# Kernel optimization log

Measured on AMD Instinct MI355X. Metric: run time of the kernel, lower is better.

## Reference

```python
import jax, jax.numpy as jnp
import numpy as np
import math

DIM = 512
D_STATE = 16
D_CONV = 4
EXPAND = 2
D_INNER = EXPAND * DIM
DT_RANK = math.ceil(DIM / 16)  # 'auto'
B_SZ = 4
N_TOK = 4097


def setup_inputs() -> dict:
    key = jax.random.key(0)
    ks = jax.random.split(key, 12)
    s = 0.02
    x = jax.random.normal(ks[0], (B_SZ, N_TOK, DIM), dtype=jnp.float32)
    q_w = jax.random.normal(ks[1], (DIM, DIM), dtype=jnp.float32) * s
    in_proj_w = jax.random.normal(ks[2], (2 * D_INNER, DIM), dtype=jnp.float32) * s
    conv_w = jax.random.normal(ks[3], (D_INNER, D_CONV), dtype=jnp.float32) * s
    conv_b = jnp.zeros((D_INNER,), dtype=jnp.float32)
    x_proj_w = jax.random.normal(ks[4], (DT_RANK + 2 * D_STATE, D_INNER), dtype=jnp.float32) * s
    dt_w = jax.random.normal(ks[5], (D_INNER, DT_RANK), dtype=jnp.float32) * (DT_RANK ** -0.5)
    # dt bias: inverse softplus of dt sampled log-uniform in [dt_min, dt_max]
    dt = jnp.exp(jax.random.uniform(ks[6], (D_INNER,)) * (math.log(0.1) - math.log(0.001)) + math.log(0.001))
    dt_b = (dt + jnp.log(-jnp.expm1(-dt))).astype(jnp.float32)
    # A = 1..d_state per channel (S4D-real init)
    A_log = jnp.log(jnp.broadcast_to(jnp.arange(1, D_STATE + 1, dtype=jnp.float32), (D_INNER, D_STATE)))
    D = jnp.ones((D_INNER,), dtype=jnp.float32)
    out_proj_w = jax.random.normal(ks[7], (DIM, D_INNER), dtype=jnp.float32) * s
    proj_w = jax.random.normal(ks[8], (DIM, DIM), dtype=jnp.float32) * s
    proj_b = jnp.zeros((DIM,), dtype=jnp.float32)
    return {"x": x, "q_w": q_w, "in_proj_w": in_proj_w, "conv_w": conv_w, "conv_b": conv_b,
            "x_proj_w": x_proj_w, "dt_w": dt_w, "dt_b": dt_b, "A_log": A_log, "D": D,
            "out_proj_w": out_proj_w, "proj_w": proj_w, "proj_b": proj_b}


def _selective_scan(u, delta, A, Bm, Cm, D):
    # u, delta: (B, L, d); A: (d, n); Bm, Cm: (B, L, n); D: (d,)
    b, L, d = u.shape
    n = A.shape[1]

    def step(h, inp):
        u_t, d_t, b_t, c_t = inp  # (B,d) (B,d) (B,n) (B,n)
        dA = jnp.exp(d_t[..., None] * A)                      # (B, d, n)
        h = h * dA + (d_t * u_t)[..., None] * b_t[:, None, :]  # (B, d, n)
        y = jnp.einsum('bdn,bn->bd', h, c_t)
        return h, y

    h0 = jnp.zeros((b, d, n), dtype=u.dtype)
    _, ys = jax.lax.scan(step, h0, (u.transpose(1, 0, 2), delta.transpose(1, 0, 2),
                                    Bm.transpose(1, 0, 2), Cm.transpose(1, 0, 2)))
    return ys.transpose(1, 0, 2) + u * D  # (B, L, d)


def _mamba(tokens, in_proj_w, conv_w, conv_b, x_proj_w, dt_w, dt_b, A_log, D, out_proj_w):
    b, L, _ = tokens.shape
    xz = tokens @ in_proj_w.T                          # (B, L, 2*d_inner)
    xi, z = jnp.split(xz, 2, axis=-1)
    # causal depthwise conv1d over L
    xc = xi.transpose(0, 2, 1)                         # (B, d_inner, L)
    xc = jax.lax.conv_general_dilated(
        xc, conv_w[:, None, :], window_strides=(1,), padding=[(D_CONV - 1, 0)],
        feature_group_count=D_INNER)
    xc = xc + conv_b[None, :, None]
    xs = jax.nn.silu(xc.transpose(0, 2, 1))            # (B, L, d_inner)
    x_dbl = xs @ x_proj_w.T                            # (B, L, dt_rank + 2n)
    dt, Bm, Cm = jnp.split(x_dbl, [DT_RANK, DT_RANK + D_STATE], axis=-1)
    delta = jax.nn.softplus(dt @ dt_w.T + dt_b)        # (B, L, d_inner)
    A = -jnp.exp(A_log)                                # (d_inner, n)
    y = _selective_scan(xs, delta, A, Bm, Cm, D)
    y = y * jax.nn.silu(z)
    return y @ out_proj_w.T                            # (B, L, dim)


def reference(x, q_w, in_proj_w, conv_w, conv_b, x_proj_w, dt_w, dt_b, A_log, D, out_proj_w, proj_w, proj_b):
    cls_tok = x[:, :1, :]
    patch = x[:, 1:, :]
    q = cls_tok @ q_w.T
    tokens = jnp.concatenate([q, patch], axis=1)
    mixed = _mamba(tokens, in_proj_w, conv_w, conv_b, x_proj_w, dt_w, dt_b, A_log, D, out_proj_w)
    upd_cls = mixed[:, :1, :] @ proj_w.T + proj_b
    return jnp.concatenate([upd_cls, patch], axis=1)
```

## Files before the change

kernel.cpp:

```cpp
#include <hip/hip_runtime.h>
#include <math.h>


#define B_SZ 4
#define DIM 512
#define D_INNER 1024
#define L_TOK 4097
#define TOK_STRIDE (L_TOK * DIM)
#define PB4 (TOK_STRIDE / 4)
#define N4 (B_SZ * PB4)
#define DT_RANK 32
#define D_STATE 16
#define CB 1639

#define SL0 0u
#define SL1 419533u
#define SL2 839066u
#define SL3 1258599u
#define SL4 1678132u
#define SL5 2097664u

__device__ __forceinline__ float silu_f(float v) { return v / (1.f + expf(-v)); }
__device__ __forceinline__ float f4dot(float4 a, float4 b) {
    return a.x * b.x + a.y * b.y + a.z * b.z + a.w * b.w;
}
__device__ __forceinline__ float red16(float v) {
    v += __shfl_xor(v, 1, 64); v += __shfl_xor(v, 2, 64);
    v += __shfl_xor(v, 4, 64); v += __shfl_xor(v, 8, 64);
    return v;
}
__device__ __forceinline__ float red32(float v) {
    v = red16(v); v += __shfl_xor(v, 16, 64); return v;
}
__device__ __forceinline__ float sel4(int c, float a0, float a1, float a2, float a3) {
    return (c == 0) ? a0 : (c == 1) ? a1 : (c == 2) ? a2 : a3;
}

__device__ __forceinline__ void do_copy(const float4* __restrict__ x4,
                                        float4* __restrict__ o4,
                                        int cb_idx, unsigned beg, unsigned end) {
    const unsigned stride = (unsigned)CB * 256u;
    for (unsigned i = beg + (unsigned)cb_idx * 256u + threadIdx.x; i < end; i += stride) {
        unsigned r = i;
        if (r >= 2u * PB4) r -= 2u * PB4;
        if (r >= (unsigned)PB4) r -= (unsigned)PB4;
        if (r >= 128u) o4[i] = x4[i];
    }
}

__global__ void __launch_bounds__(256)
k1_q(const float* __restrict__ x, const float* __restrict__ q_w,
     float* __restrict__ q_ws, float4* __restrict__ o4) {
    const int blk = blockIdx.x, tid = threadIdx.x;
    if (blk >= 8) { do_copy((const float4*)x, o4, blk - 8, SL0, SL1); return; }
    __shared__ float cls[4 * DIM];
    {
        float4* cl4 = (float4*)cls;
        const float4* xg = (const float4*)x;
#pragma unroll
        for (int t = 0; t < 2; ++t) {
            int f = tid + t * 256;
            cl4[f] = xg[(size_t)(f >> 7) * PB4 + (f & 127)];
        }
    }
    __syncthreads();
    const int w = tid >> 6, lane = tid & 63, c = lane & 15, g = lane >> 4;
#pragma unroll
    for (int p = 0; p < 4; ++p) {
        int r = blk * 64 + w * 16 + p * 4 + g;
        const float4* wr = (const float4*)(q_w + (size_t)r * DIM);
        float a0 = 0, a1 = 0, a2 = 0, a3 = 0;
#pragma unroll
        for (int j = 0; j < 8; ++j) {
            float4 wv = wr[c + 16 * j];
            a0 += f4dot(wv, ((const float4*)(cls))[c + 16 * j]);
            a1 += f4dot(wv, ((const float4*)(cls + DIM))[c + 16 * j]);
            a2 += f4dot(wv, ((const float4*)(cls + 2 * DIM))[c + 16 * j]);
            a3 += f4dot(wv, ((const float4*)(cls + 3 * DIM))[c + 16 * j]);
        }
        a0 = red16(a0); a1 = red16(a1); a2 = red16(a2); a3 = red16(a3);
        if (c < 4) q_ws[c * DIM + r] = sel4(c, a0, a1, a2, a3);
    }
}

__global__ void __launch_bounds__(256)
k2_xz(const float* __restrict__ q_ws, const float* __restrict__ in_proj_w,
      const float* __restrict__ conv_w, const float* __restrict__ conv_b,
      float* __restrict__ xs_ws, float* __restrict__ gz_ws,
      const float4* __restrict__ x4, float4* __restrict__ o4) {
    const int blk = blockIdx.x, tid = threadIdx.x;
    if (blk >= 32) { do_copy(x4, o4, blk - 32, SL1, SL2); return; }
    __shared__ float q_lds[4 * DIM];
    {
        float4* ql = (float4*)q_lds;
        const float4* qg = (const float4*)q_ws;
        ql[tid] = qg[tid]; ql[tid + 256] = qg[tid + 256];
    }
    __syncthreads();
    const int w = tid >> 6, lane = tid & 63, c = lane & 15, g = lane >> 4;
#pragma unroll
    for (int p = 0; p < 4; ++p) {
        int r = blk * 64 + w * 16 + p * 4 + g;
        const float4* wr = (const float4*)(in_proj_w + (size_t)r * DIM);
        float a0 = 0, a1 = 0, a2 = 0, a3 = 0;
#pragma unroll
        for (int j = 0; j < 8; ++j) {
            float4 wv = wr[c + 16 * j];
            a0 += f4dot(wv, ((const float4*)(q_lds))[c + 16 * j]);
            a1 += f4dot(wv, ((const float4*)(q_lds + DIM))[c + 16 * j]);
            a2 += f4dot(wv, ((const float4*)(q_lds + 2 * DIM))[c + 16 * j]);
            a3 += f4dot(wv, ((const float4*)(q_lds + 3 * DIM))[c + 16 * j]);
        }
        a0 = red16(a0); a1 = red16(a1); a2 = red16(a2); a3 = red16(a3);
        if (c < 4) {
            float v = sel4(c, a0, a1, a2, a3);
            if (r < D_INNER)
                xs_ws[c * D_INNER + r] = silu_f(v * conv_w[r * 4 + 3] + conv_b[r]);
            else
                gz_ws[c * D_INNER + (r - D_INNER)] = silu_f(v);
        }
    }
}

__global__ void __launch_bounds__(256)
k3_xd(const float* __restrict__ xs_ws, const float* __restrict__ x_proj_w,
      float* __restrict__ xd_ws, const float4* __restrict__ x4,
      float4* __restrict__ o4) {
    const int blk = blockIdx.x, tid = threadIdx.x;
    if (blk >= 4) { do_copy(x4, o4, blk - 4, SL2, SL3); return; }
    __shared__ float xs_lds[4 * D_INNER];
    {
        float4* xl = (float4*)xs_lds;
        const float4* xg = (const float4*)xs_ws;
#pragma unroll
        for (int t = 0; t < 4; ++t) xl[tid + t * 256] = xg[tid + t * 256];
    }
    __syncthreads();
    const int w = tid >> 6, lane = tid & 63, c2 = lane & 31, g2 = lane >> 5;
#pragma unroll
    for (int p = 0; p < 2; ++p) {
        int r = blk * 16 + w * 4 + p * 2 + g2;
        const float4* wr = (const float4*)(x_proj_w + (size_t)r * D_INNER);
        float a0 = 0, a1 = 0, a2 = 0, a3 = 0;
#pragma unroll
        for (int j = 0; j < 8; ++j) {
            float4 wv = wr[c2 + 32 * j];
            a0 += f4dot(wv, ((const float4*)(xs_lds))[c2 + 32 * j]);
            a1 += f4dot(wv, ((const float4*)(xs_lds + D_INNER))[c2 + 32 * j]);
            a2 += f4dot(wv, ((const float4*)(xs_lds + 2 * D_INNER))[c2 + 32 * j]);
            a3 += f4dot(wv, ((const float4*)(xs_lds + 3 * D_INNER))[c2 + 32 * j]);
        }
        a0 = red32(a0); a1 = red32(a1); a2 = red32(a2); a3 = red32(a3);
        if (c2 < 4) xd_ws[c2 * 64 + r] = sel4(c2, a0, a1, a2, a3);
    }
}

__global__ void __launch_bounds__(256)
k4_out(const float* __restrict__ xs_ws, const float* __restrict__ gz_ws,
       const float* __restrict__ xd_ws, const float* __restrict__ dt_w,
       const float* __restrict__ dt_b, const float* __restrict__ Dp,
       const float* __restrict__ out_proj_w, float* __restrict__ o_ws,
       const float4* __restrict__ x4, float4* __restrict__ o4) {
    const int blk = blockIdx.x, tid = threadIdx.x;
    if (blk >= 16) { do_copy(x4, o4, blk - 16, SL3, SL4); return; }
    __shared__ float xd_lds[4 * 64];
    __shared__ float y_lds[4 * D_INNER];
    if (tid < 64) ((float4*)xd_lds)[tid] = ((const float4*)xd_ws)[tid];
    __syncthreads();
    float S[4];
#pragma unroll
    for (int b = 0; b < 4; ++b) {
        float s = 0.f;
#pragma unroll
        for (int n = 0; n < D_STATE; ++n)
            s += xd_lds[b * 64 + 32 + n] * xd_lds[b * 64 + 48 + n];
        S[b] = s;
    }
#pragma unroll
    for (int qq = 0; qq < 4; ++qq) {
        int d = tid + qq * 256;
        const float4* dw = (const float4*)(dt_w + (size_t)d * DT_RANK);
        float4 dwv[8];
#pragma unroll
        for (int j = 0; j < 8; ++j) dwv[j] = dw[j];
        float Dd = Dp[d], db = dt_b[d];
#pragma unroll
        for (int b = 0; b < 4; ++b) {
            const float4* xd4 = (const float4*)(xd_lds + b * 64);
            float dp = db;
#pragma unroll
            for (int j = 0; j < 8; ++j) dp += f4dot(dwv[j], xd4[j]);
            float delta = (dp > 20.f) ? dp : log1pf(expf(dp));
            y_lds[b * D_INNER + d] =
                xs_ws[b * D_INNER + d] * (delta * S[b] + Dd) * gz_ws[b * D_INNER + d];
        }
    }
    __syncthreads();
    const int w = tid >> 6, lane = tid & 63, c2 = lane & 31, g2 = lane >> 5;
#pragma unroll
    for (int p = 0; p < 4; ++p) {
        int r = blk * 32 + w * 8 + p * 2 + g2;
        const float4* wr = (const float4*)(out_proj_w + (size_t)r * D_INNER);
        float a0 = 0, a1 = 0, a2 = 0, a3 = 0;
#pragma unroll
        for (int j = 0; j < 8; ++j) {
            float4 wv = wr[c2 + 32 * j];
            a0 += f4dot(wv, ((const float4*)(y_lds))[c2 + 32 * j]);
            a1 += f4dot(wv, ((const float4*)(y_lds + D_INNER))[c2 + 32 * j]);
            a2 += f4dot(wv, ((const float4*)(y_lds + 2 * D_INNER))[c2 + 32 * j]);
            a3 += f4dot(wv, ((const float4*)(y_lds + 3 * D_INNER))[c2 + 32 * j]);
        }
        a0 = red32(a0); a1 = red32(a1); a2 = red32(a2); a3 = red32(a3);
        if (c2 < 4) o_ws[c2 * DIM + r] = sel4(c2, a0, a1, a2, a3);
    }
}

__global__ void __launch_bounds__(256)
k5_upd(const float* __restrict__ o_ws, const float* __restrict__ proj_w,
       const float* __restrict__ proj_b, float* __restrict__ out,
       const float4* __restrict__ x4, float4* __restrict__ o4) {
    const int blk = blockIdx.x, tid = threadIdx.x;
    if (blk >= 8) { do_copy(x4, o4, blk - 8, SL4, SL5); return; }
    __shared__ float o_lds[4 * DIM];
    {
        float4* ol = (float4*)o_lds;
        const float4* og = (const float4*)o_ws;
        ol[tid] = og[tid]; ol[tid + 256] = og[tid + 256];
    }
    __syncthreads();
    const int w = tid >> 6, lane = tid & 63, c = lane & 15, g = lane >> 4;
#pragma unroll
    for (int p = 0; p < 4; ++p) {
        int r = blk * 64 + w * 16 + p * 4 + g;
        const float4* wr = (const float4*)(proj_w + (size_t)r * DIM);
        float a0 = 0, a1 = 0, a2 = 0, a3 = 0;
#pragma unroll
        for (int j = 0; j < 8; ++j) {
            float4 wv = wr[c + 16 * j];
            a0 += f4dot(wv, ((const float4*)(o_lds))[c + 16 * j]);
            a1 += f4dot(wv, ((const float4*)(o_lds + DIM))[c + 16 * j]);
            a2 += f4dot(wv, ((const float4*)(o_lds + 2 * DIM))[c + 16 * j]);
            a3 += f4dot(wv, ((const float4*)(o_lds + 3 * DIM))[c + 16 * j]);
        }
        a0 = red16(a0); a1 = red16(a1); a2 = red16(a2); a3 = red16(a3);
        if (c < 4) out[(size_t)c * TOK_STRIDE + r] = sel4(c, a0, a1, a2, a3) + proj_b[r];
    }
}

extern "C" void kernel_launch(void* const* d_in, const int* in_sizes, int n_in,
                              void* d_out, int out_size, void* d_ws, size_t ws_size,
                              hipStream_t stream) {
    const float* x          = (const float*)d_in[0];
    const float* q_w        = (const float*)d_in[1];
    const float* in_proj_w  = (const float*)d_in[2];
    const float* conv_w     = (const float*)d_in[3];
    const float* conv_b     = (const float*)d_in[4];
    const float* x_proj_w   = (const float*)d_in[5];
    const float* dt_w       = (const float*)d_in[6];
    const float* dt_b       = (const float*)d_in[7];
    const float* Dp         = (const float*)d_in[9];
    const float* out_proj_w = (const float*)d_in[10];
    const float* proj_w     = (const float*)d_in[11];
    const float* proj_b     = (const float*)d_in[12];
    float* out = (float*)d_out;
    float* ws  = (float*)d_ws;

    float* q_ws  = ws;
    float* xs_ws = ws + 2048;
    float* gz_ws = ws + 6144;
    float* xd_ws = ws + 10240;
    float* o_ws  = ws + 10496;

    const float4* x4 = (const float4*)x;
    float4* o4 = (float4*)out;

    k1_q  <<<8 + CB,  256, 0, stream>>>(x, q_w, q_ws, o4);
    k2_xz <<<32 + CB, 256, 0, stream>>>(q_ws, in_proj_w, conv_w, conv_b,
                                        xs_ws, gz_ws, x4, o4);
    k3_xd <<<4 + CB,  256, 0, stream>>>(xs_ws, x_proj_w, xd_ws, x4, o4);
    k4_out<<<16 + CB, 256, 0, stream>>>(xs_ws, gz_ws, xd_ws, dt_w, dt_b, Dp,
                                        out_proj_w, o_ws, x4, o4);
    k5_upd<<<8 + CB,  256, 0, stream>>>(o_ws, proj_w, proj_b, out, x4, o4);
}
```

Measured before the change: 146.8 us.

## Fuse x_proj stage into out-projection kernel, redundantly per block

Removes the separate x_proj kernel launch by having each of the 16 out-projection blocks recompute the full 64-row x_proj product from LDS-resident xs. The background patch copy is repartitioned into four slices instead of five, with a larger copy-block count per launch. This trades one fewer launch and a global round-trip for redundant x_proj work in every compute block and larger LDS use per block.

```diff
diff --git a/kernel.cpp b/kernel.cpp
--- a/kernel.cpp
+++ b/kernel.cpp
@@ -8,17 +8,15 @@
 #define L_TOK 4097
 #define TOK_STRIDE (L_TOK * DIM)
 #define PB4 (TOK_STRIDE / 4)
-#define N4 (B_SZ * PB4)
 #define DT_RANK 32
 #define D_STATE 16
-#define CB 1639
+#define CB 2040
 
 #define SL0 0u
-#define SL1 419533u
-#define SL2 839066u
-#define SL3 1258599u
-#define SL4 1678132u
-#define SL5 2097664u
+#define SL1 ((unsigned)PB4)
+#define SL2 (2u * PB4)
+#define SL3 (3u * PB4)
+#define SL4 (4u * PB4)
 
 __device__ __forceinline__ float silu_f(float v) { return v / (1.f + expf(-v)); }
 __device__ __forceinline__ float f4dot(float4 a, float4 b) {
@@ -123,12 +121,16 @@
 }
 
 __global__ void __launch_bounds__(256)
-k3_xd(const float* __restrict__ xs_ws, const float* __restrict__ x_proj_w,
-      float* __restrict__ xd_ws, const float4* __restrict__ x4,
-      float4* __restrict__ o4) {
-    const int blk = blockIdx.x, tid = threadIdx.x;
-    if (blk >= 4) { do_copy(x4, o4, blk - 4, SL2, SL3); return; }
+k4_out(const float* __restrict__ xs_ws, const float* __restrict__ gz_ws,
+       const float* __restrict__ x_proj_w, const float* __restrict__ dt_w,
+       const float* __restrict__ dt_b, const float* __restrict__ Dp,
+       const float* __restrict__ out_proj_w, float* __restrict__ o_ws,
+       const float4* __restrict__ x4, float4* __restrict__ o4) {
+    const int blk = blockIdx.x, tid = threadIdx.x;
+    if (blk >= 16) { do_copy(x4, o4, blk - 16, SL2, SL3); return; }
     __shared__ float xs_lds[4 * D_INNER];
+    __shared__ float xd_lds[4 * 64];
+    __shared__ float y_lds[4 * D_INNER];
     {
         float4* xl = (float4*)xs_lds;
         const float4* xg = (const float4*)xs_ws;
@@ -137,9 +139,10 @@
     }
     __syncthreads();
     const int w = tid >> 6, lane = tid & 63, c2 = lane & 31, g2 = lane >> 5;
-#pragma unroll
-    for (int p = 0; p < 2; ++p) {
-        int r = blk * 16 + w * 4 + p * 2 + g2;
+
+#pragma unroll
+    for (int p = 0; p < 8; ++p) {
+        int r = p * 8 + w * 2 + g2;
         const float4* wr = (const float4*)(x_proj_w + (size_t)r * D_INNER);
         float a0 = 0, a1 = 0, a2 = 0, a3 = 0;
 #pragma unroll
@@ -151,22 +154,10 @@
             a3 += f4dot(wv, ((const float4*)(xs_lds + 3 * D_INNER))[c2 + 32 * j]);
         }
         a0 = red32(a0); a1 = red32(a1); a2 = red32(a2); a3 = red32(a3);
-        if (c2 < 4) xd_ws[c2 * 64 + r] = sel4(c2, a0, a1, a2, a3);
-    }
-}
-
-__global__ void __launch_bounds__(256)
-k4_out(const float* __restrict__ xs_ws, const float* __restrict__ gz_ws,
-       const float* __restrict__ xd_ws, const float* __restrict__ dt_w,
-       const float* __restrict__ dt_b, const float* __restrict__ Dp,
-       const float* __restrict__ out_proj_w, float* __restrict__ o_ws,
-       const float4* __restrict__ x4, float4* __restrict__ o4) {
-    const int blk = blockIdx.x, tid = threadIdx.x;
-    if (blk >= 16) { do_copy(x4, o4, blk - 16, SL3, SL4); return; }
-    __shared__ float xd_lds[4 * 64];
-    __shared__ float y_lds[4 * D_INNER];
-    if (tid < 64) ((float4*)xd_lds)[tid] = ((const float4*)xd_ws)[tid];
-    __syncthreads();
+        if (c2 < 4) xd_lds[c2 * 64 + r] = sel4(c2, a0, a1, a2, a3);
+    }
+    __syncthreads();
+
     float S[4];
 #pragma unroll
     for (int b = 0; b < 4; ++b) {
@@ -192,11 +183,11 @@
             for (int j = 0; j < 8; ++j) dp += f4dot(dwv[j], xd4[j]);
             float delta = (dp > 20.f) ? dp : log1pf(expf(dp));
             y_lds[b * D_INNER + d] =
-                xs_ws[b * D_INNER + d] * (delta * S[b] + Dd) * gz_ws[b * D_INNER + d];
-        }
-    }
-    __syncthreads();
-    const int w = tid >> 6, lane = tid & 63, c2 = lane & 31, g2 = lane >> 5;
+                xs_lds[b * D_INNER + d] * (delta * S[b] + Dd) * gz_ws[b * D_INNER + d];
+        }
+    }
+    __syncthreads();
+
 #pragma unroll
     for (int p = 0; p < 4; ++p) {
         int r = blk * 32 + w * 8 + p * 2 + g2;
@@ -220,7 +211,7 @@
        const float* __restrict__ proj_b, float* __restrict__ out,
        const float4* __restrict__ x4, float4* __restrict__ o4) {
     const int blk = blockIdx.x, tid = threadIdx.x;
-    if (blk >= 8) { do_copy(x4, o4, blk - 8, SL4, SL5); return; }
+    if (blk >= 8) { do_copy(x4, o4, blk - 8, SL3, SL4); return; }
     __shared__ float o_lds[4 * DIM];
     {
         float4* ol = (float4*)o_lds;
@@ -268,8 +259,7 @@
     float* q_ws  = ws;
     float* xs_ws = ws + 2048;
     float* gz_ws = ws + 6144;
-    float* xd_ws = ws + 10240;
-    float* o_ws  = ws + 10496;
+    float* o_ws  = ws + 10240;
 
     const float4* x4 = (const float4*)x;
     float4* o4 = (float4*)out;
@@ -277,8 +267,7 @@
     k1_q  <<<8 + CB,  256, 0, stream>>>(x, q_w, q_ws, o4);
     k2_xz <<<32 + CB, 256, 0, stream>>>(q_ws, in_proj_w, conv_w, conv_b,
                                         xs_ws, gz_ws, x4, o4);
-    k3_xd <<<4 + CB,  256, 0, stream>>>(xs_ws, x_proj_w, xd_ws, x4, o4);
-    k4_out<<<16 + CB, 256, 0, stream>>>(xs_ws, gz_ws, xd_ws, dt_w, dt_b, Dp,
+    k4_out<<<16 + CB, 256, 0, stream>>>(xs_ws, gz_ws, x_proj_w, dt_w, dt_b, Dp,
                                         out_proj_w, o_ws, x4, o4);
     k5_upd<<<8 + CB,  256, 0, stream>>>(o_ws, proj_w, proj_b, out, x4, o4);
 }
```

Result: slower. 152.4 us (+3.8%).
